# Kernel tuning notes

Hardware: AMD Instinct MI355X
Metric: run time of the kernel (lower is better)

Reference implementation:

```python
import jax, jax.numpy as jnp
import numpy as np

EPS = 1e-5
HEADS = 4
RES = 28          # resolution H = W
PS = 14           # patch_size (pooled grid side)
POOL = RES // PS  # patch_pool_size = 2


def _local_init_pos_w():
    # Deterministic local init (locality_strength=1.0); kernel_size = sqrt(num_heads) = 2
    ks = int(HEADS ** 0.5)
    center = (ks - 1) / 2 if ks % 2 == 0 else ks // 2
    w = np.zeros((HEADS, 3), dtype=np.float32)
    for h1 in range(ks):
        for h2 in range(ks):
            pos = h1 + ks * h2
            w[pos, 2] = -1.0
            w[pos, 1] = 2.0 * (h1 - center)
            w[pos, 0] = 2.0 * (h2 - center)
    return jnp.asarray(w)


def setup_inputs() -> dict:
    key = jax.random.key(0)
    B, T, C = 32, RES * RES, 768
    x = jax.random.normal(key, (B, T, C), dtype=jnp.float32)
    return {
        "x": x,
        "weight": jnp.ones((C,), jnp.float32),
        "bias": jnp.zeros((C,), jnp.float32),
        "mean_norm_weight": jnp.zeros((HEADS,), jnp.float32),
        "var_norm_weight": jnp.zeros((HEADS,), jnp.float32),
        "pos_w": _local_init_pos_w(),
        "pos_b": jnp.zeros((HEADS,), jnp.float32),
    }


def _rel_indices(ps, dtype):
    # (P, P, 3) relative position features: [indx, indy, indx^2 + indy^2]
    ind = jnp.arange(ps)[None, :] - jnp.arange(ps)[:, None]  # (ps, ps)
    indx = jnp.tile(ind, (ps, ps))                            # (P, P)
    indy = jnp.repeat(jnp.repeat(ind, ps, axis=0), ps, axis=1)
    return jnp.stack([indx, indy, indx * indx + indy * indy], axis=-1).astype(dtype)


def reference(x, weight, bias, mean_norm_weight, var_norm_weight, pos_w, pos_b):
    B, T, C = x.shape
    Ch = C // HEADS
    P = PS * PS

    # group "moment2" normalization
    g = x.reshape(B, T, HEADS, Ch)
    m2 = jnp.mean(g * g, axis=3, keepdims=True)
    xn = (g / jnp.sqrt(m2 + EPS)).reshape(B, T, C)

    mw = jax.nn.sigmoid(mean_norm_weight)  # (HEADS,)
    vw = jax.nn.sigmoid(var_norm_weight)

    # position scores: Linear(3 -> heads) then softmax over source-patch axis
    rel = _rel_indices(PS, x.dtype)                 # (P, P, 3)
    scores = rel @ pos_w.T + pos_b                  # (P, P, HEADS)
    pos = jax.nn.softmax(scores, axis=0)            # softmax over dim -2 of (B,h,i,j)
    pos_h = jnp.transpose(pos, (2, 0, 1))           # (HEADS, P, P)

    mean_ln = xn.mean(axis=2)                       # (B, T)
    var_ln = xn.var(axis=2, ddof=1)                 # torch unbiased var

    # spatialize + avg-pool POOLxPOOL
    xs = xn.reshape(B, RES, RES, C).transpose(0, 3, 1, 2)          # (B, C, 28, 28)
    xp = xs.reshape(B, C, PS, POOL, PS, POOL).mean(axis=(3, 5))    # (B, C, 14, 14)
    xp = xp.reshape(B, HEADS, Ch, P)

    mean_r = jnp.einsum('bhci,hij->bhcj', xp, pos_h)
    mean2_r = jnp.einsum('bhci,hij->bhcj', xp * xp, pos_h)
    var_r = mean2_r - mean_r * mean_r

    def unpool(y):  # nearest-neighbor upsample back to T tokens
        y = y.reshape(B, HEADS, Ch, PS, PS)
        y = jnp.broadcast_to(y[:, :, :, :, None, :, None],
                             (B, HEADS, Ch, PS, POOL, PS, POOL))
        return y.reshape(B, HEADS, Ch, T)

    mean_r = unpool(mean_r)
    var_r = unpool(var_r)

    mwv = mw.reshape(1, HEADS, 1, 1)
    vwv = vw.reshape(1, HEADS, 1, 1)
    mean_r = (1.0 - mwv) * mean_r + mwv * mean_ln[:, None, None, :]
    var_r = (1.0 - vwv) * var_r + vwv * var_ln[:, None, None, :]

    mean_r = mean_r.reshape(B, C, T).transpose(0, 2, 1)  # (B, T, C)
    var_r = var_r.reshape(B, C, T).transpose(0, 2, 1)

    out = (xn - mean_r) / jnp.sqrt(var_r + EPS)
    return out * weight.reshape(1, 1, C) + bias.reshape(1, 1, C)
```

## Files before the change

kernel.cpp:

```cpp
#include <hip/hip_runtime.h>

#define NB   32
#define NT   784
#define NC   768
#define NH   4
#define CH   192
#define PSZ  14
#define NP   196
#define RESO 28
#define EPSV 1e-5f

__global__ __launch_bounds__(256) void k_norm_pool(
    const float* __restrict__ x,
    float* __restrict__ inv_m2, float* __restrict__ mean_ln,
    float* __restrict__ var_ln, float4* __restrict__ xp4) {
  __shared__ float4 xl4[4 * 192];
  int bid = blockIdx.x;
  int b = bid / NP, ip = bid % NP;
  int pr = ip / PSZ, pc = ip % PSZ;
  int tid = threadIdx.x;
  int k = tid >> 6, lane = tid & 63;
  int t = (2 * pr + (k >> 1)) * RESO + (2 * pc + (k & 1));

  const float4* row = (const float4*)(x + (size_t)(b * NT + t) * NC);
  int f4b = (lane >> 4) * 48 + (lane & 15) * 3;
  float4 v0 = row[f4b], v1 = row[f4b + 1], v2 = row[f4b + 2];

  float d = v0.x * v0.x + v0.y * v0.y + v0.z * v0.z + v0.w * v0.w +
            v1.x * v1.x + v1.y * v1.y + v1.z * v1.z + v1.w * v1.w +
            v2.x * v2.x + v2.y * v2.y + v2.z * v2.z + v2.w * v2.w;
#pragma unroll
  for (int s = 1; s <= 8; s <<= 1) d += __shfl_xor(d, s, 64);
  float iv = rsqrtf(d * (1.f / CH) + EPSV);
  if ((lane & 15) == 0)
    inv_m2[(size_t)(b * NT + t) * NH + (lane >> 4)] = iv;

  v0.x *= iv; v0.y *= iv; v0.z *= iv; v0.w *= iv;
  v1.x *= iv; v1.y *= iv; v1.z *= iv; v1.w *= iv;
  v2.x *= iv; v2.y *= iv; v2.z *= iv; v2.w *= iv;

  float sm = v0.x + v0.y + v0.z + v0.w + v1.x + v1.y + v1.z + v1.w +
             v2.x + v2.y + v2.z + v2.w;
  float sq = v0.x * v0.x + v0.y * v0.y + v0.z * v0.z + v0.w * v0.w +
             v1.x * v1.x + v1.y * v1.y + v1.z * v1.z + v1.w * v1.w +
             v2.x * v2.x + v2.y * v2.y + v2.z * v2.z + v2.w * v2.w;
#pragma unroll
  for (int s = 1; s <= 32; s <<= 1) {
    sm += __shfl_xor(sm, s, 64);
    sq += __shfl_xor(sq, s, 64);
  }
  if (lane == 0) {
    float mean = sm / (float)NC;
    mean_ln[b * NT + t] = mean;
    var_ln[b * NT + t] = (sq - (float)NC * mean * mean) / (float)(NC - 1);
  }

  xl4[k * 192 + f4b]     = v0;
  xl4[k * 192 + f4b + 1] = v1;
  xl4[k * 192 + f4b + 2] = v2;
  __syncthreads();

  if (tid < 192) {
    float4 a = xl4[tid], bb = xl4[192 + tid], c = xl4[384 + tid], dd = xl4[576 + tid];
    float4 r;
    r.x = (a.x + bb.x + c.x + dd.x) * 0.25f;
    r.y = (a.y + bb.y + c.y + dd.y) * 0.25f;
    r.z = (a.z + bb.z + c.z + dd.z) * 0.25f;
    r.w = (a.w + bb.w + c.w + dd.w) * 0.25f;
    xp4[(size_t)(b * NP + ip) * 192 + tid] = r;
  }
}

__global__ __launch_bounds__(256) void k_fused(
    const float* __restrict__ xp, const float* __restrict__ pos_w,
    const float* __restrict__ mnw, const float* __restrict__ vnw,
    const float* __restrict__ x,
    const float* __restrict__ weight, const float* __restrict__ bias,
    const float* __restrict__ inv_m2, const float* __restrict__ mean_ln,
    const float* __restrict__ var_ln, float* __restrict__ out) {
  __shared__ float fns[NH * PSZ];
  __shared__ float gns[NH * PSZ * PSZ];
  __shared__ float tstat[4 * PSZ][6];
  __shared__ float sgate[8];

  int bid0 = blockIdx.x;
  int bid = (bid0 & 7) * 168 + (bid0 >> 3);
  int b = bid / 42, r = bid % 42;
  int s = r / PSZ, jx = r % PSZ;
  int tid = threadIdx.x;
  int h = tid >> 6, lane = tid & 63;
  int c = h * CH + s * 64 + lane;

  if (tid < NH * PSZ) {
    int hh = tid / PSZ, jr = tid % PSZ;
    float w1 = pos_w[hh * 3 + 1], w2 = pos_w[hh * 3 + 2];
    float e[PSZ], mx = -1e30f;
#pragma unroll
    for (int i = 0; i < PSZ; ++i) {
      float dd = (float)(jr - i);
      float sc = w1 * dd + w2 * dd * dd;
      e[i] = sc; mx = fmaxf(mx, sc);
    }
    float sum = 0.f;
#pragma unroll
    for (int i = 0; i < PSZ; ++i) { e[i] = expf(e[i] - mx); sum += e[i]; }
    float invs = 1.f / sum;
#pragma unroll
    for (int i = 0; i < PSZ; ++i) gns[(hh * PSZ + jr) * PSZ + i] = e[i] * invs;
  }
  if (tid >= 64 && tid < 64 + NH) {
    int hh = tid - 64;
    float w0 = pos_w[hh * 3 + 0], w2 = pos_w[hh * 3 + 2];
    float e[PSZ], mx = -1e30f;
#pragma unroll
    for (int i = 0; i < PSZ; ++i) {
      float dd = (float)(jx - i);
      float sc = w0 * dd + w2 * dd * dd;
      e[i] = sc; mx = fmaxf(mx, sc);
    }
    float sum = 0.f;
#pragma unroll
    for (int i = 0; i < PSZ; ++i) { e[i] = expf(e[i] - mx); sum += e[i]; }
    float invs = 1.f / sum;
#pragma unroll
    for (int i = 0; i < PSZ; ++i) fns[hh * PSZ + i] = e[i] * invs;
  }
  if (tid >= 72 && tid < 80) {
    int g = tid - 72;
    float v = (g < 4) ? mnw[g] : vnw[g - 4];
    sgate[g] = 1.f / (1.f + expf(-v));
  }
  for (int idx = tid; idx < 4 * PSZ * 6; idx += 256) {
    int l = idx / 6, f = idx % 6;
    int jy = l >> 2, kk = l & 3;
    int t = (2 * jy + (kk >> 1)) * RESO + (2 * jx + (kk & 1));
    size_t o = (size_t)(b * NT + t);
    tstat[l][f] = (f < 4) ? inv_m2[o * NH + f]
                : (f == 4) ? mean_ln[o] : var_ln[o];
  }
  __syncthreads();

  float t1[PSZ], t2[PSZ];
#pragma unroll
  for (int iy = 0; iy < PSZ; ++iy) { t1[iy] = 0.f; t2[iy] = 0.f; }

  const float* base = xp + (size_t)b * NP * NC + c;
#pragma unroll
  for (int iy = 0; iy < PSZ; ++iy) {
    const float* prow = base + (size_t)(iy * PSZ) * NC;
#pragma unroll
    for (int ix = 0; ix < PSZ; ++ix) {
      float f = fns[h * PSZ + ix];
      float v = prow[ix * NC];
      t1[iy] += f * v;
      t2[iy] += f * (v * v);
    }
  }

  float wv = weight[c], bv = bias[c];
  float mw = sgate[h], vw = sgate[4 + h];
  float omw = 1.f - mw, ovw = 1.f - vw;
  const float* gh = &gns[h * NP];

#pragma unroll 1
  for (int jy = 0; jy < PSZ; ++jy) {
    float m = 0.f, q = 0.f;
#pragma unroll
    for (int iy = 0; iy < PSZ; ++iy) {
      float g = gh[jy * PSZ + iy];
      m += g * t1[iy];
      q += g * t2[iy];
    }
    float p = fmaxf(q - m * m, 0.f);
    float mb = omw * m, vb = ovw * p;

#pragma unroll
    for (int kk = 0; kk < 4; ++kk) {
      int t = (2 * jy + (kk >> 1)) * RESO + (2 * jx + (kk & 1));
      size_t xo = (size_t)(b * NT + t) * NC;
      int l = jy * 4 + kk;
      float ivv = tstat[l][h];
      float ml = tstat[l][4], vl = tstat[l][5];

      float xn = x[xo + c] * ivv;
      float mr = mb + mw * ml;
      float vr = vb + vw * vl;
      out[xo + c] = (xn - mr) * rsqrtf(vr + EPSV) * wv + bv;
    }
  }
}

extern "C" void kernel_launch(void* const* d_in, const int* in_sizes, int n_in,
                              void* d_out, int out_size, void* d_ws, size_t ws_size,
                              hipStream_t stream) {
  const float* x     = (const float*)d_in[0];
  const float* wgt   = (const float*)d_in[1];
  const float* bias  = (const float*)d_in[2];
  const float* mnw   = (const float*)d_in[3];
  const float* vnw   = (const float*)d_in[4];
  const float* pos_w = (const float*)d_in[5];
  float* out = (float*)d_out;

  float* ws      = (float*)d_ws;
  float* inv_m2  = ws;
  float* mean_ln = inv_m2 + (size_t)NB * NT * NH;
  float* var_ln  = mean_ln + (size_t)NB * NT;
  float* xp      = var_ln + (size_t)NB * NT;

  hipLaunchKernelGGL(k_norm_pool, dim3(NB * NP), dim3(256), 0, stream,
                     x, inv_m2, mean_ln, var_ln, (float4*)xp);
  hipLaunchKernelGGL(k_fused, dim3(NB * 3 * PSZ), dim3(256), 0, stream,
                     xp, pos_w, mnw, vnw, x, wgt, bias, inv_m2, mean_ln, var_ln, out);
}
```

Baseline: 177.3 us.

## Process two pooled columns per block to reuse pooled-tile loads

Each k_fused block now handles two jx columns instead of one, so every pooled value read from xp feeds both columns' row-reduction accumulators. This halves the redundant xp reads, which were 196 loads per thread repeated for every column, and halves the block count. In exchange it doubles accumulator registers (56 floats), which may lower occupancy, and leaves only 672 blocks on the GPU.

```diff
diff --git a/kernel.cpp b/kernel.cpp
--- a/kernel.cpp
+++ b/kernel.cpp
@@ -9,6 +9,8 @@
 #define NP   196
 #define RESO 28
 #define EPSV 1e-5f
+#define JXB  2
+#define NJT  (PSZ / JXB)
 
 __global__ __launch_bounds__(256) void k_norm_pool(
     const float* __restrict__ x,
@@ -78,15 +80,16 @@
     const float* __restrict__ weight, const float* __restrict__ bias,
     const float* __restrict__ inv_m2, const float* __restrict__ mean_ln,
     const float* __restrict__ var_ln, float* __restrict__ out) {
-  __shared__ float fns[NH * PSZ];
+  __shared__ float fns[JXB][NH * PSZ];
   __shared__ float gns[NH * PSZ * PSZ];
-  __shared__ float tstat[4 * PSZ][6];
+  __shared__ float tstat[JXB][4 * PSZ][6];
   __shared__ float sgate[8];
 
   int bid0 = blockIdx.x;
-  int bid = (bid0 & 7) * 168 + (bid0 >> 3);
-  int b = bid / 42, r = bid % 42;
-  int s = r / PSZ, jx = r % PSZ;
+  int bid = (bid0 & 7) * 84 + (bid0 >> 3);
+  int b = bid / (3 * NJT), r = bid % (3 * NJT);
+  int s = r / NJT, jt = r % NJT;
+  int jx0 = jt * JXB;
   int tid = threadIdx.x;
   int h = tid >> 6, lane = tid & 63;
   int c = h * CH + s * 64 + lane;
@@ -108,13 +111,15 @@
 #pragma unroll
     for (int i = 0; i < PSZ; ++i) gns[(hh * PSZ + jr) * PSZ + i] = e[i] * invs;
   }
-  if (tid >= 64 && tid < 64 + NH) {
-    int hh = tid - 64;
+  if (tid >= 64 && tid < 64 + JXB * NH) {
+    int idx = tid - 64;
+    int jj = idx >> 2, hh = idx & 3;
+    int jxx = jx0 + jj;
     float w0 = pos_w[hh * 3 + 0], w2 = pos_w[hh * 3 + 2];
     float e[PSZ], mx = -1e30f;
 #pragma unroll
     for (int i = 0; i < PSZ; ++i) {
-      float dd = (float)(jx - i);
+      float dd = (float)(jxx - i);
       float sc = w0 * dd + w2 * dd * dd;
       e[i] = sc; mx = fmaxf(mx, sc);
     }
@@ -123,37 +128,42 @@
     for (int i = 0; i < PSZ; ++i) { e[i] = expf(e[i] - mx); sum += e[i]; }
     float invs = 1.f / sum;
 #pragma unroll
-    for (int i = 0; i < PSZ; ++i) fns[hh * PSZ + i] = e[i] * invs;
+    for (int i = 0; i < PSZ; ++i) fns[jj][hh * PSZ + i] = e[i] * invs;
   }
   if (tid >= 72 && tid < 80) {
     int g = tid - 72;
     float v = (g < 4) ? mnw[g] : vnw[g - 4];
     sgate[g] = 1.f / (1.f + expf(-v));
   }
-  for (int idx = tid; idx < 4 * PSZ * 6; idx += 256) {
-    int l = idx / 6, f = idx % 6;
+  for (int idx = tid; idx < JXB * 4 * PSZ * 6; idx += 256) {
+    int jj = idx / (4 * PSZ * 6), rem = idx % (4 * PSZ * 6);
+    int l = rem / 6, f = rem % 6;
     int jy = l >> 2, kk = l & 3;
-    int t = (2 * jy + (kk >> 1)) * RESO + (2 * jx + (kk & 1));
+    int jxx = jx0 + jj;
+    int t = (2 * jy + (kk >> 1)) * RESO + (2 * jxx + (kk & 1));
     size_t o = (size_t)(b * NT + t);
-    tstat[l][f] = (f < 4) ? inv_m2[o * NH + f]
-                : (f == 4) ? mean_ln[o] : var_ln[o];
+    tstat[jj][l][f] = (f < 4) ? inv_m2[o * NH + f]
+                    : (f == 4) ? mean_ln[o] : var_ln[o];
   }
   __syncthreads();
 
-  float t1[PSZ], t2[PSZ];
-#pragma unroll
-  for (int iy = 0; iy < PSZ; ++iy) { t1[iy] = 0.f; t2[iy] = 0.f; }
+  float t1[JXB][PSZ], t2[JXB][PSZ];
+#pragma unroll
+  for (int jj = 0; jj < JXB; ++jj)
+#pragma unroll
+    for (int iy = 0; iy < PSZ; ++iy) { t1[jj][iy] = 0.f; t2[jj][iy] = 0.f; }
 
   const float* base = xp + (size_t)b * NP * NC + c;
 #pragma unroll
-  for (int iy = 0; iy < PSZ; ++iy) {
-    const float* prow = base + (size_t)(iy * PSZ) * NC;
-#pragma unroll
-    for (int ix = 0; ix < PSZ; ++ix) {
-      float f = fns[h * PSZ + ix];
-      float v = prow[ix * NC];
-      t1[iy] += f * v;
-      t2[iy] += f * (v * v);
+  for (int ix = 0; ix < PSZ; ++ix) {
+    float fA = fns[0][h * PSZ + ix];
+    float fB = fns[1][h * PSZ + ix];
+#pragma unroll
+    for (int iy = 0; iy < PSZ; ++iy) {
+      float v = base[(size_t)(iy * PSZ + ix) * NC];
+      float vv = v * v;
+      t1[0][iy] += fA * v;  t2[0][iy] += fA * vv;
+      t1[1][iy] += fB * v;  t2[1][iy] += fB * vv;
     }
   }
 
@@ -162,30 +172,34 @@
   float omw = 1.f - mw, ovw = 1.f - vw;
   const float* gh = &gns[h * NP];
 
+#pragma unroll
+  for (int jj = 0; jj < JXB; ++jj) {
+    int jxx = jx0 + jj;
 #pragma unroll 1
-  for (int jy = 0; jy < PSZ; ++jy) {
-    float m = 0.f, q = 0.f;
-#pragma unroll
-    for (int iy = 0; iy < PSZ; ++iy) {
-      float g = gh[jy * PSZ + iy];
-      m += g * t1[iy];
-      q += g * t2[iy];
-    }
-    float p = fmaxf(q - m * m, 0.f);
-    float mb = omw * m, vb = ovw * p;
-
-#pragma unroll
-    for (int kk = 0; kk < 4; ++kk) {
-      int t = (2 * jy + (kk >> 1)) * RESO + (2 * jx + (kk & 1));
-      size_t xo = (size_t)(b * NT + t) * NC;
-      int l = jy * 4 + kk;
-      float ivv = tstat[l][h];
-      float ml = tstat[l][4], vl = tstat[l][5];
-
-      float xn = x[xo + c] * ivv;
-      float mr = mb + mw * ml;
-      float vr = vb + vw * vl;
-      out[xo + c] = (xn - mr) * rsqrtf(vr + EPSV) * wv + bv;
+    for (int jy = 0; jy < PSZ; ++jy) {
+      float m = 0.f, q = 0.f;
+#pragma unroll
+      for (int iy = 0; iy < PSZ; ++iy) {
+        float g = gh[jy * PSZ + iy];
+        m += g * t1[jj][iy];
+        q += g * t2[jj][iy];
+      }
+      float p = fmaxf(q - m * m, 0.f);
+      float mb = omw * m, vb = ovw * p;
+
+#pragma unroll
+      for (int kk = 0; kk < 4; ++kk) {
+        int t = (2 * jy + (kk >> 1)) * RESO + (2 * jxx + (kk & 1));
+        size_t xo = (size_t)(b * NT + t) * NC;
+        int l = jy * 4 + kk;
+        float ivv = tstat[jj][l][h];
+        float ml = tstat[jj][l][4], vl = tstat[jj][l][5];
+
+        float xn = x[xo + c] * ivv;
+        float mr = mb + mw * ml;
+        float vr = vb + vw * vl;
+        out[xo + c] = (xn - mr) * rsqrtf(vr + EPSV) * wv + bv;
+      }
     }
   }
 }
@@ -209,6 +223,6 @@
 
   hipLaunchKernelGGL(k_norm_pool, dim3(NB * NP), dim3(256), 0, stream,
                      x, inv_m2, mean_ln, var_ln, (float4*)xp);
-  hipLaunchKernelGGL(k_fused, dim3(NB * 3 * PSZ), dim3(256), 0, stream,
+  hipLaunchKernelGGL(k_fused, dim3(NB * 3 * NJT), dim3(256), 0, stream,
                      xp, pos_w, mnw, vnw, x, wgt, bias, inv_m2, mean_ln, var_ln, out);
 }
```

Result: slower. 232.7 us (+31.3%).

## Vectorize fused kernel to float4 per thread covering all channels per block

Applied to the files above, without the earlier changes.

Each thread in the fused kernel now handles four consecutive channels with float4 loads and stores. A 192-thread block therefore covers all 768 channels for one (batch, column) pair, so the grid shrinks from 1344 to 448 blocks. This cuts the number of memory instructions and the per-block setup cost (softmax tables, token stats), which was repeated three times per column. In exchange each thread keeps four times as many accumulator registers (56 floats per accumulator array), which lowers occupancy, and fewer blocks may underfill the 256 CUs.

```diff
diff --git a/kernel.cpp b/kernel.cpp
--- a/kernel.cpp
+++ b/kernel.cpp
@@ -9,6 +9,7 @@
 #define NP   196
 #define RESO 28
 #define EPSV 1e-5f
+#define NSL  192
 
 __global__ __launch_bounds__(256) void k_norm_pool(
     const float* __restrict__ x,
@@ -71,25 +72,23 @@
   }
 }
 
-__global__ __launch_bounds__(256) void k_fused(
-    const float* __restrict__ xp, const float* __restrict__ pos_w,
+__global__ __launch_bounds__(192) void k_fused(
+    const float4* __restrict__ xp4, const float* __restrict__ pos_w,
     const float* __restrict__ mnw, const float* __restrict__ vnw,
-    const float* __restrict__ x,
-    const float* __restrict__ weight, const float* __restrict__ bias,
+    const float4* __restrict__ x4,
+    const float4* __restrict__ weight4, const float4* __restrict__ bias4,
     const float* __restrict__ inv_m2, const float* __restrict__ mean_ln,
-    const float* __restrict__ var_ln, float* __restrict__ out) {
+    const float* __restrict__ var_ln, float4* __restrict__ out4) {
   __shared__ float fns[NH * PSZ];
   __shared__ float gns[NH * PSZ * PSZ];
   __shared__ float tstat[4 * PSZ][6];
   __shared__ float sgate[8];
 
   int bid0 = blockIdx.x;
-  int bid = (bid0 & 7) * 168 + (bid0 >> 3);
-  int b = bid / 42, r = bid % 42;
-  int s = r / PSZ, jx = r % PSZ;
+  int bid = (bid0 & 7) * 56 + (bid0 >> 3);
+  int b = bid / PSZ, jx = bid % PSZ;
   int tid = threadIdx.x;
-  int h = tid >> 6, lane = tid & 63;
-  int c = h * CH + s * 64 + lane;
+  int h = tid / 48;
 
   if (tid < NH * PSZ) {
     int hh = tid / PSZ, jr = tid % PSZ;
@@ -130,7 +129,7 @@
     float v = (g < 4) ? mnw[g] : vnw[g - 4];
     sgate[g] = 1.f / (1.f + expf(-v));
   }
-  for (int idx = tid; idx < 4 * PSZ * 6; idx += 256) {
+  for (int idx = tid; idx < 4 * PSZ * 6; idx += 192) {
     int l = idx / 6, f = idx % 6;
     int jy = l >> 2, kk = l & 3;
     int t = (2 * jy + (kk >> 1)) * RESO + (2 * jx + (kk & 1));
@@ -140,52 +139,71 @@
   }
   __syncthreads();
 
-  float t1[PSZ], t2[PSZ];
-#pragma unroll
-  for (int iy = 0; iy < PSZ; ++iy) { t1[iy] = 0.f; t2[iy] = 0.f; }
-
-  const float* base = xp + (size_t)b * NP * NC + c;
+  float4 t1[PSZ], t2[PSZ];
 #pragma unroll
   for (int iy = 0; iy < PSZ; ++iy) {
-    const float* prow = base + (size_t)(iy * PSZ) * NC;
+    t1[iy].x = t1[iy].y = t1[iy].z = t1[iy].w = 0.f;
+    t2[iy].x = t2[iy].y = t2[iy].z = t2[iy].w = 0.f;
+  }
+
+  const float4* base = xp4 + (size_t)b * NP * NSL + tid;
+#pragma unroll
+  for (int iy = 0; iy < PSZ; ++iy) {
 #pragma unroll
     for (int ix = 0; ix < PSZ; ++ix) {
       float f = fns[h * PSZ + ix];
-      float v = prow[ix * NC];
-      t1[iy] += f * v;
-      t2[iy] += f * (v * v);
-    }
-  }
-
-  float wv = weight[c], bv = bias[c];
+      float4 v = base[(size_t)(iy * PSZ + ix) * NSL];
+      float ax = f * v.x, ay = f * v.y, az = f * v.z, aw = f * v.w;
+      t1[iy].x += ax;        t1[iy].y += ay;
+      t1[iy].z += az;        t1[iy].w += aw;
+      t2[iy].x += ax * v.x;  t2[iy].y += ay * v.y;
+      t2[iy].z += az * v.z;  t2[iy].w += aw * v.w;
+    }
+  }
+
+  float4 wv = weight4[tid], bv = bias4[tid];
   float mw = sgate[h], vw = sgate[4 + h];
   float omw = 1.f - mw, ovw = 1.f - vw;
   const float* gh = &gns[h * NP];
+  const float4* xb = x4 + (size_t)b * NT * NSL + tid;
+  float4* ob = out4 + (size_t)b * NT * NSL + tid;
 
 #pragma unroll 1
   for (int jy = 0; jy < PSZ; ++jy) {
-    float m = 0.f, q = 0.f;
+    float4 m, q;
+    m.x = m.y = m.z = m.w = 0.f;
+    q.x = q.y = q.z = q.w = 0.f;
 #pragma unroll
     for (int iy = 0; iy < PSZ; ++iy) {
       float g = gh[jy * PSZ + iy];
-      m += g * t1[iy];
-      q += g * t2[iy];
-    }
-    float p = fmaxf(q - m * m, 0.f);
-    float mb = omw * m, vb = ovw * p;
+      m.x += g * t1[iy].x; m.y += g * t1[iy].y;
+      m.z += g * t1[iy].z; m.w += g * t1[iy].w;
+      q.x += g * t2[iy].x; q.y += g * t2[iy].y;
+      q.z += g * t2[iy].z; q.w += g * t2[iy].w;
+    }
+    float4 mb, vb;
+    mb.x = omw * m.x; mb.y = omw * m.y; mb.z = omw * m.z; mb.w = omw * m.w;
+    vb.x = ovw * fmaxf(q.x - m.x * m.x, 0.f);
+    vb.y = ovw * fmaxf(q.y - m.y * m.y, 0.f);
+    vb.z = ovw * fmaxf(q.z - m.z * m.z, 0.f);
+    vb.w = ovw * fmaxf(q.w - m.w * m.w, 0.f);
 
 #pragma unroll
     for (int kk = 0; kk < 4; ++kk) {
       int t = (2 * jy + (kk >> 1)) * RESO + (2 * jx + (kk & 1));
-      size_t xo = (size_t)(b * NT + t) * NC;
       int l = jy * 4 + kk;
       float ivv = tstat[l][h];
       float ml = tstat[l][4], vl = tstat[l][5];
-
-      float xn = x[xo + c] * ivv;
-      float mr = mb + mw * ml;
-      float vr = vb + vw * vl;
-      out[xo + c] = (xn - mr) * rsqrtf(vr + EPSV) * wv + bv;
+      float mr = mw * ml;
+      float vr = vw * vl + EPSV;
+
+      float4 xv = xb[(size_t)t * NSL];
+      float4 r;
+      r.x = (xv.x * ivv - (mb.x + mr)) * rsqrtf(vb.x + vr) * wv.x + bv.x;
+      r.y = (xv.y * ivv - (mb.y + mr)) * rsqrtf(vb.y + vr) * wv.y + bv.y;
+      r.z = (xv.z * ivv - (mb.z + mr)) * rsqrtf(vb.z + vr) * wv.z + bv.z;
+      r.w = (xv.w * ivv - (mb.w + mr)) * rsqrtf(vb.w + vr) * wv.w + bv.w;
+      ob[(size_t)t * NSL] = r;
     }
   }
 }
@@ -209,6 +227,8 @@
 
   hipLaunchKernelGGL(k_norm_pool, dim3(NB * NP), dim3(256), 0, stream,
                      x, inv_m2, mean_ln, var_ln, (float4*)xp);
-  hipLaunchKernelGGL(k_fused, dim3(NB * 3 * PSZ), dim3(256), 0, stream,
-                     xp, pos_w, mnw, vnw, x, wgt, bias, inv_m2, mean_ln, var_ln, out);
+  hipLaunchKernelGGL(k_fused, dim3(NB * PSZ), dim3(192), 0, stream,
+                     (const float4*)xp, pos_w, mnw, vnw, (const float4*)x,
+                     (const float4*)wgt, (const float4*)bias,
+                     inv_m2, mean_ln, var_ln, (float4*)out);
 }
```

Result: slower. 213.7 us (+20.5%).

## Restructure fused kernel to tile 32-channel slices with pooled data staged in LDS

Applied to the files above, without the earlier changes.

The fused kernel now assigns each block one batch and one 32-channel slice within a single head, with 448 threads covering all 14 output columns. The whole pooled slice (196 patches × 32 channels) and the per-token stats for all 784 tokens are staged in shared memory once. Before, each block re-read pooled data from global memory for a single column, so the same pooled data was fetched many times. The cost is 32-channel-wide accesses to x and out (128-byte segments instead of 256), larger LDS use that lowers occupancy, and a smaller grid of 768 blocks.

```diff
diff --git a/kernel.cpp b/kernel.cpp
--- a/kernel.cpp
+++ b/kernel.cpp
@@ -9,6 +9,9 @@
 #define NP   196
 #define RESO 28
 #define EPSV 1e-5f
+#define CSL  32
+#define NSLC (NC / CSL)
+#define BTH  448
 
 __global__ __launch_bounds__(256) void k_norm_pool(
     const float* __restrict__ x,
@@ -71,29 +74,47 @@
   }
 }
 
-__global__ __launch_bounds__(256) void k_fused(
-    const float* __restrict__ xp, const float* __restrict__ pos_w,
+__global__ __launch_bounds__(BTH) void k_fused(
+    const float4* __restrict__ xp4, const float* __restrict__ pos_w,
     const float* __restrict__ mnw, const float* __restrict__ vnw,
     const float* __restrict__ x,
     const float* __restrict__ weight, const float* __restrict__ bias,
     const float* __restrict__ inv_m2, const float* __restrict__ mean_ln,
     const float* __restrict__ var_ln, float* __restrict__ out) {
-  __shared__ float fns[NH * PSZ];
-  __shared__ float gns[NH * PSZ * PSZ];
-  __shared__ float tstat[4 * PSZ][6];
-  __shared__ float sgate[8];
+  __shared__ float4 sxp4[NP * (CSL / 4)];
+  __shared__ float sF[PSZ * PSZ];
+  __shared__ float sG[PSZ * PSZ];
+  __shared__ float tstat[NT][3];
 
   int bid0 = blockIdx.x;
-  int bid = (bid0 & 7) * 168 + (bid0 >> 3);
-  int b = bid / 42, r = bid % 42;
-  int s = r / PSZ, jx = r % PSZ;
+  int bidS = (bid0 & 7) * 96 + (bid0 >> 3);
+  int b = bidS / NSLC, s = bidS % NSLC;
+  int hs = s / 6;
   int tid = threadIdx.x;
-  int h = tid >> 6, lane = tid & 63;
-  int c = h * CH + s * 64 + lane;
-
-  if (tid < NH * PSZ) {
-    int hh = tid / PSZ, jr = tid % PSZ;
-    float w1 = pos_w[hh * 3 + 1], w2 = pos_w[hh * 3 + 2];
+  int jx = tid >> 5;
+  int ch = tid & 31;
+  int c = s * CSL + ch;
+
+  if (tid < PSZ) {
+    int jf = tid;
+    float w0 = pos_w[hs * 3 + 0], w2 = pos_w[hs * 3 + 2];
+    float e[PSZ], mx = -1e30f;
+#pragma unroll
+    for (int i = 0; i < PSZ; ++i) {
+      float dd = (float)(jf - i);
+      float sc = w0 * dd + w2 * dd * dd;
+      e[i] = sc; mx = fmaxf(mx, sc);
+    }
+    float sum = 0.f;
+#pragma unroll
+    for (int i = 0; i < PSZ; ++i) { e[i] = expf(e[i] - mx); sum += e[i]; }
+    float invs = 1.f / sum;
+#pragma unroll
+    for (int i = 0; i < PSZ; ++i) sF[jf * PSZ + i] = e[i] * invs;
+  }
+  if (tid >= 64 && tid < 64 + PSZ) {
+    int jr = tid - 64;
+    float w1 = pos_w[hs * 3 + 1], w2 = pos_w[hs * 3 + 2];
     float e[PSZ], mx = -1e30f;
 #pragma unroll
     for (int i = 0; i < PSZ; ++i) {
@@ -106,68 +127,52 @@
     for (int i = 0; i < PSZ; ++i) { e[i] = expf(e[i] - mx); sum += e[i]; }
     float invs = 1.f / sum;
 #pragma unroll
-    for (int i = 0; i < PSZ; ++i) gns[(hh * PSZ + jr) * PSZ + i] = e[i] * invs;
-  }
-  if (tid >= 64 && tid < 64 + NH) {
-    int hh = tid - 64;
-    float w0 = pos_w[hh * 3 + 0], w2 = pos_w[hh * 3 + 2];
-    float e[PSZ], mx = -1e30f;
-#pragma unroll
-    for (int i = 0; i < PSZ; ++i) {
-      float dd = (float)(jx - i);
-      float sc = w0 * dd + w2 * dd * dd;
-      e[i] = sc; mx = fmaxf(mx, sc);
-    }
-    float sum = 0.f;
-#pragma unroll
-    for (int i = 0; i < PSZ; ++i) { e[i] = expf(e[i] - mx); sum += e[i]; }
-    float invs = 1.f / sum;
-#pragma unroll
-    for (int i = 0; i < PSZ; ++i) fns[hh * PSZ + i] = e[i] * invs;
-  }
-  if (tid >= 72 && tid < 80) {
-    int g = tid - 72;
-    float v = (g < 4) ? mnw[g] : vnw[g - 4];
-    sgate[g] = 1.f / (1.f + expf(-v));
-  }
-  for (int idx = tid; idx < 4 * PSZ * 6; idx += 256) {
-    int l = idx / 6, f = idx % 6;
-    int jy = l >> 2, kk = l & 3;
-    int t = (2 * jy + (kk >> 1)) * RESO + (2 * jx + (kk & 1));
-    size_t o = (size_t)(b * NT + t);
-    tstat[l][f] = (f < 4) ? inv_m2[o * NH + f]
-                : (f == 4) ? mean_ln[o] : var_ln[o];
-  }
+    for (int i = 0; i < PSZ; ++i) sG[jr * PSZ + i] = e[i] * invs;
+  }
+
+  {
+    const float4* src = xp4 + (size_t)b * NP * (NC / 4) + s * (CSL / 4);
+    for (int i = tid; i < NP * (CSL / 4); i += BTH) {
+      int p = i >> 3, q = i & 7;
+      sxp4[i] = src[(size_t)p * (NC / 4) + q];
+    }
+  }
+  for (int i = tid; i < NT; i += BTH) {
+    size_t o = (size_t)(b * NT + i);
+    tstat[i][0] = inv_m2[o * NH + hs];
+    tstat[i][1] = mean_ln[o];
+    tstat[i][2] = var_ln[o];
+  }
+
+  float mw = 1.f / (1.f + expf(-mnw[hs]));
+  float vw = 1.f / (1.f + expf(-vnw[hs]));
+  float omw = 1.f - mw, ovw = 1.f - vw;
+  float wv = weight[c], bv = bias[c];
+
   __syncthreads();
 
   float t1[PSZ], t2[PSZ];
 #pragma unroll
   for (int iy = 0; iy < PSZ; ++iy) { t1[iy] = 0.f; t2[iy] = 0.f; }
 
-  const float* base = xp + (size_t)b * NP * NC + c;
+  const float* sx = (const float*)sxp4;
 #pragma unroll
   for (int iy = 0; iy < PSZ; ++iy) {
-    const float* prow = base + (size_t)(iy * PSZ) * NC;
 #pragma unroll
     for (int ix = 0; ix < PSZ; ++ix) {
-      float f = fns[h * PSZ + ix];
-      float v = prow[ix * NC];
+      float f = sF[jx * PSZ + ix];
+      float v = sx[(iy * PSZ + ix) * CSL + ch];
       t1[iy] += f * v;
       t2[iy] += f * (v * v);
     }
   }
-
-  float wv = weight[c], bv = bias[c];
-  float mw = sgate[h], vw = sgate[4 + h];
-  float omw = 1.f - mw, ovw = 1.f - vw;
-  const float* gh = &gns[h * NP];
 
 #pragma unroll 1
   for (int jy = 0; jy < PSZ; ++jy) {
     float m = 0.f, q = 0.f;
 #pragma unroll
     for (int iy = 0; iy < PSZ; ++iy) {
-      float g = gh[jy * PSZ + iy];
+      float g = sG[jy * PSZ + iy];
       m += g * t1[iy];
       q += g * t2[iy];
     }
@@ -177,15 +182,14 @@
 #pragma unroll
     for (int kk = 0; kk < 4; ++kk) {
       int t = (2 * jy + (kk >> 1)) * RESO + (2 * jx + (kk & 1));
-      size_t xo = (size_t)(b * NT + t) * NC;
-      int l = jy * 4 + kk;
-      float ivv = tstat[l][h];
-      float ml = tstat[l][4], vl = tstat[l][5];
-
-      float xn = x[xo + c] * ivv;
+      size_t xo = (size_t)(b * NT + t) * NC + c;
+      float ivv = tstat[t][0];
+      float ml  = tstat[t][1], vl = tstat[t][2];
+
+      float xn = x[xo] * ivv;
       float mr = mb + mw * ml;
       float vr = vb + vw * vl;
-      out[xo + c] = (xn - mr) * rsqrtf(vr + EPSV) * wv + bv;
+      out[xo] = (xn - mr) * rsqrtf(vr + EPSV) * wv + bv;
     }
   }
 }
@@ -209,6 +213,7 @@
 
   hipLaunchKernelGGL(k_norm_pool, dim3(NB * NP), dim3(256), 0, stream,
                      x, inv_m2, mean_ln, var_ln, (float4*)xp);
-  hipLaunchKernelGGL(k_fused, dim3(NB * 3 * PSZ), dim3(256), 0, stream,
-                     xp, pos_w, mnw, vnw, x, wgt, bias, inv_m2, mean_ln, var_ln, out);
+  hipLaunchKernelGGL(k_fused, dim3(NB * NSLC), dim3(BTH), 0, stream,
+                     (const float4*)xp, pos_w, mnw, vnw, x, wgt, bias,
+                     inv_m2, mean_ln, var_ln, out);
 }
```

After: 168.5 us. -4.9%, faster.
